# Kernel tuning notes

Measured on AMD Instinct MI355X. Metric: run time of the kernel, lower is better.

The kernel has to match this reference:

```python
import jax, jax.numpy as jnp
import numpy as np

B = 8
A = 3
LEVEL_HW = [(200, 304), (100, 152), (50, 76), (25, 38), (13, 19)]
LEVEL_SIZES = [A * h * w for h, w in LEVEL_HW]  # anchors per level
N_TOTAL = sum(LEVEL_SIZES)                      # 242991
IMG_H, IMG_W = 800.0, 1216.0
PRE_NMS_TOP_N = 2000
POST_NMS_TOP_N = 100
NMS_THRESH = 0.7
MIN_SIZE = 1e-3
BBOX_XFORM_CLIP = float(np.log(1000.0 / 16.0))
NEG = -1e30


def setup_inputs() -> dict:
    key = jax.random.key(0)
    ks = jax.random.split(key, 2 * len(LEVEL_HW) + 3)
    inp = {}
    for i, (h, w) in enumerate(LEVEL_HW):
        inp[f"cls{i}"] = jax.random.normal(ks[2 * i], (B, A, h, w), dtype=jnp.float32)
        inp[f"box{i}"] = jax.random.normal(ks[2 * i + 1], (B, 4 * A, h, w), dtype=jnp.float32) * 0.5
    kc, kw, _ = ks[-3], ks[-2], ks[-1]
    c = jax.random.uniform(kc, (N_TOTAL, 2), dtype=jnp.float32) * jnp.array([IMG_W, IMG_H], jnp.float32)
    wh = 16.0 + jax.random.uniform(kw, (N_TOTAL, 2), dtype=jnp.float32) * 240.0
    inp["anchors"] = jnp.concatenate([c - 0.5 * wh, c + 0.5 * wh], axis=-1)  # x1y1x2y2
    return inp


def _permute_flatten(p, C):
    # [N, A*C, H, W] -> [N, H*W*A, C]  (matches permute_and_flatten)
    n, ac, h, w = p.shape
    a = ac // C
    return p.reshape(n, a, C, h, w).transpose(0, 3, 4, 1, 2).reshape(n, -1, C)


def _decode(deltas, anchors):
    wa = anchors[:, 2] - anchors[:, 0]
    ha = anchors[:, 3] - anchors[:, 1]
    cxa = anchors[:, 0] + 0.5 * wa
    cya = anchors[:, 1] + 0.5 * ha
    dx, dy = deltas[..., 0], deltas[..., 1]
    dw = jnp.minimum(deltas[..., 2], BBOX_XFORM_CLIP)
    dh = jnp.minimum(deltas[..., 3], BBOX_XFORM_CLIP)
    cx = dx * wa + cxa
    cy = dy * ha + cya
    pw = jnp.exp(dw) * wa
    ph = jnp.exp(dh) * ha
    return jnp.stack([cx - 0.5 * pw, cy - 0.5 * ph, cx + 0.5 * pw, cy + 0.5 * ph], axis=-1)


def _nms_single(boxes, scores, lvl, valid):
    # batched_nms: offset boxes by level so cross-level boxes never overlap
    off = lvl.astype(boxes.dtype)[:, None] * (max(IMG_H, IMG_W) + 1.0)
    b0 = boxes + off
    s0 = jnp.where(valid, scores, NEG)  # small-box removal -> impossible to pick
    order = jnp.argsort(-s0)
    b = b0[order]
    s = s0[order]
    areas = (b[:, 2] - b[:, 0]) * (b[:, 3] - b[:, 1])
    suppressed0 = s <= NEG / 2
    idx_range = jnp.arange(s.shape[0])

    def step(suppressed, _):
        avail = jnp.where(suppressed, NEG, s)
        i = jnp.argmax(avail)
        ok = avail[i] > NEG / 2
        bi = b[i]
        xx1 = jnp.maximum(b[:, 0], bi[0])
        yy1 = jnp.maximum(b[:, 1], bi[1])
        xx2 = jnp.minimum(b[:, 2], bi[2])
        yy2 = jnp.minimum(b[:, 3], bi[3])
        inter = jnp.maximum(xx2 - xx1, 0.0) * jnp.maximum(yy2 - yy1, 0.0)
        union = areas + areas[i] - inter
        iou = jnp.where(union > 0, inter / union, 0.0)
        sup_new = suppressed | (iou > NMS_THRESH) | (idx_range == i)
        return jnp.where(ok, sup_new, suppressed), (jnp.where(ok, order[i], 0), ok)

    _, (sel, selv) = jax.lax.scan(step, suppressed0, None, length=POST_NMS_TOP_N)
    out_boxes = jnp.where(selv[:, None], boxes[sel], 0.0)
    out_scores = jnp.where(selv, scores[sel], 0.0)
    return out_boxes, out_scores


def reference(cls0, cls1, cls2, cls3, cls4, box0, box1, box2, box3, box4, anchors):
    cls_levels = [cls0, cls1, cls2, cls3, cls4]
    box_levels = [box0, box1, box2, box3, box4]
    pred_class = jnp.concatenate([_permute_flatten(c, 1) for c in cls_levels], axis=1)  # [B,N,1]
    deltas = jnp.concatenate([_permute_flatten(b, 4) for b in box_levels], axis=1)      # [B,N,4]
    proposals = _decode(deltas, anchors)                                               # [B,N,4]
    scores = pred_class[..., 0]                                                        # [B,N]

    # per-level top-k; replicates the original's cumulative k = min(k, num_anchor)
    keep, lvl = [], []
    k, off = PRE_NMS_TOP_N, 0
    for li, n in enumerate(LEVEL_SIZES):
        k = min(k, n)
        _, idx = jax.lax.top_k(scores[:, off:off + n], k)
        keep.append(idx + off)
        lvl.append(jnp.full((k,), li, dtype=jnp.int32))
        off += n
    keep = jnp.concatenate(keep, axis=1)   # [B,K]
    lvl = jnp.concatenate(lvl)             # [K]

    prop = jnp.take_along_axis(proposals, keep[..., None], axis=1)  # [B,K,4]
    sc = jnp.take_along_axis(scores, keep, axis=1)                  # [B,K]
    prop = jnp.stack([
        jnp.clip(prop[..., 0], 0.0, IMG_W), jnp.clip(prop[..., 1], 0.0, IMG_H),
        jnp.clip(prop[..., 2], 0.0, IMG_W), jnp.clip(prop[..., 3], 0.0, IMG_H)], axis=-1)
    valid = ((prop[..., 2] - prop[..., 0]) >= MIN_SIZE) & ((prop[..., 3] - prop[..., 1]) >= MIN_SIZE)
    boxes_out, scores_out = jax.vmap(lambda bx, s, v: _nms_single(bx, s, lvl, v))(prop, sc, valid)
    return boxes_out, scores_out  # [B,100,4], [B,100]
```

## Files before the change

### kernel.cpp

```cpp
#include <hip/hip_runtime.h>
#include <cstdint>

#define NTOT 242991
#define BATCH 8
#define KTOT 8741
#define CAP 8192
#define NBIN 4096
#define CSTR 16
#define MEMTOT 1943928
#define SLICE 256
#define RSTR 9
#define BCAP 2048
#define NB2 2048
#define DBLK 9

__device__ __forceinline__ int level_of(int n) {
    if (n < 182400) return 0;
    if (n < 228000) return 1;
    if (n < 239400) return 2;
    if (n < 242250) return 3;
    return 4;
}

__device__ __forceinline__ void locate(int n, int& l, int& H, int& W, int& loc) {
    if (n < 182400)      { l = 0; H = 200; W = 304; loc = n; }
    else if (n < 228000) { l = 1; H = 100; W = 152; loc = n - 182400; }
    else if (n < 239400) { l = 2; H = 50;  W = 76;  loc = n - 228000; }
    else if (n < 242250) { l = 3; H = 25;  W = 38;  loc = n - 239400; }
    else                 { l = 4; H = 13;  W = 19;  loc = n - 242250; }
}

__device__ __forceinline__ int classify_bl(int x) {
    int l, HW;
    if (x < 1459200)      { l = 0; HW = 60800; }
    else if (x < 1824000) { l = 1; HW = 15200; x -= 1459200; }
    else if (x < 1915200) { l = 2; HW = 3800;  x -= 1824000; }
    else if (x < 1938000) { l = 3; HW = 950;   x -= 1915200; }
    else                  { l = 4; HW = 247;   x -= 1938000; }
    return (x / (3 * HW)) * 5 + l;
}

__device__ __forceinline__ void mem_decompose(int x, int& b, int& n, int& bl) {
    int HW, off, l;
    if (x < 1459200)      { l = 0; HW = 60800; off = 0; }
    else if (x < 1824000) { l = 1; HW = 15200; off = 182400; x -= 1459200; }
    else if (x < 1915200) { l = 2; HW = 3800;  off = 228000; x -= 1824000; }
    else if (x < 1938000) { l = 3; HW = 950;   off = 239400; x -= 1915200; }
    else                  { l = 4; HW = 247;   off = 242250; x -= 1938000; }
    int seg = 3 * HW;
    b = x / seg; int r = x - b * seg;
    int a = r / HW, pix = r - a * HW;
    n = off + pix * 3 + a;
    bl = b * 5 + l;
}

__device__ __forceinline__ float read_cls(int gid, const float* c0, const float* c1,
                                          const float* c2, const float* c3, const float* c4) {
    return (gid < 1459200) ? c0[gid] :
           (gid < 1824000) ? c1[gid - 1459200] :
           (gid < 1915200) ? c2[gid - 1824000] :
           (gid < 1938000) ? c3[gid - 1915200] : c4[gid - 1938000];
}

__device__ __forceinline__ uint32_t suffix_scan_1024(uint32_t g, uint32_t* lds16, int t) {
    int lane = t & 63, wid = t >> 6;
    uint32_t v = g;
#pragma unroll
    for (int o = 1; o < 64; o <<= 1) {
        uint32_t oth = __shfl_down(v, o, 64);
        if (lane + o < 64) v += oth;
    }
    if (lane == 0) lds16[wid] = v;
    __syncthreads();
    uint32_t w = 0;
    for (int q = wid + 1; q < 16; q++) w += lds16[q];
    __syncthreads();
    return v + w;
}

__device__ __forceinline__ uint32_t prefix_scan_1024(uint32_t g, uint32_t* lds16, int t) {
    int lane = t & 63, wid = t >> 6;
    uint32_t v = g;
#pragma unroll
    for (int o = 1; o < 64; o <<= 1) {
        uint32_t oth = __shfl_up(v, o, 64);
        if (lane >= o) v += oth;
    }
    if (lane == 63) lds16[wid] = v;
    __syncthreads();
    uint32_t w = 0;
    for (int q = 0; q < wid; q++) w += lds16[q];
    __syncthreads();
    return v + w;
}

__device__ __forceinline__ bool iou_hit(float bx1, float by1, float bx2, float by2, float ca,
                                        float4 sv) {
    float xx1 = fmaxf(bx1, sv.x), yy1 = fmaxf(by1, sv.y);
    float xx2 = fminf(bx2, sv.z), yy2 = fminf(by2, sv.w);
    float inter = fmaxf(xx2 - xx1, 0.f) * fmaxf(yy2 - yy1, 0.f);
    float sa = (sv.z - sv.x) * (sv.w - sv.y);
    float un = ca + sa - inter;
    return (un > 0.f) && (inter / un > 0.7f);
}

__global__ __launch_bounds__(1024)
void k_keys(const float* __restrict__ c0, const float* __restrict__ c1,
            const float* __restrict__ c2, const float* __restrict__ c3,
            const float* __restrict__ c4, uint32_t* __restrict__ hist) {
    int t = threadIdx.x;
    int base = blockIdx.x * 1024;
    int gid = base + t;
    bool in = gid < MEMTOT;
    __shared__ uint32_t lh[NBIN];

    int bl = 0, b, n;
    uint32_t u = 0;
    if (in) {
        mem_decompose(gid, b, n, bl);
        float sv = read_cls(gid, c0, c1, c2, c3, c4);
        u = __float_as_uint(sv);
        u ^= (u >> 31) ? 0xFFFFFFFFu : 0x80000000u;
    }
    int blf = classify_bl(base);
    int bll = classify_bl(min(base + 1023, MEMTOT - 1));
    if (blf == bll) {
        for (int j = t; j < NBIN; j += 1024) lh[j] = 0u;
        __syncthreads();
        if (in) atomicAdd(&lh[u >> 20], 1u);
        __syncthreads();
        uint32_t* gh = hist + (size_t)blf * NBIN;
        for (int j = t; j < NBIN; j += 1024) {
            uint32_t v = lh[j];
            if (v) atomicAdd(&gh[j], v);
        }
    } else {
        if (in) atomicAdd(&hist[(size_t)bl * NBIN + (u >> 20)], 1u);
    }
}

__global__ void k_bins(const uint32_t* __restrict__ hist, int* __restrict__ binT,
                       int* __restrict__ rrem) {
    int bl = blockIdx.x;
    const uint32_t* h = hist + (size_t)bl * NBIN;
    int l = bl % 5;
    uint32_t k = (l == 4) ? 741u : 2000u;
    __shared__ uint32_t ts[256];
    __shared__ uint32_t sb[256];
    int t = threadIdx.x;
    uint32_t hh[16];
#pragma unroll
    for (int i = 0; i < 16; i++) hh[i] = h[t * 16 + i];
    uint32_t s = 0;
#pragma unroll
    for (int i = 0; i < 16; i++) s += hh[i];
    ts[t] = s; sb[t] = s;
    __syncthreads();
    for (int d = 1; d < 256; d <<= 1) {
        uint32_t add = (t + d < 256) ? sb[t + d] : 0u;
        __syncthreads();
        sb[t] += add;
        __syncthreads();
    }
    uint32_t inc = sb[t], excl = inc - ts[t];
    if (excl < k && inc >= k) {
        uint32_t cum = excl;
#pragma unroll
        for (int i = 15; i >= 0; i--) {
            if (cum + hh[i] >= k) { binT[bl] = t * 16 + i; rrem[bl] = (int)(k - cum); break; }
            cum += hh[i];
        }
    }
}

__global__ __launch_bounds__(1024)
void k_compact(const float* __restrict__ c0, const float* __restrict__ c1,
               const float* __restrict__ c2, const float* __restrict__ c3,
               const float* __restrict__ c4, const int* __restrict__ binT,
               uint32_t* __restrict__ keep_n, uint32_t* __restrict__ keep_u,
               uint32_t* __restrict__ keep_cnt,
               uint32_t* __restrict__ cand_n, uint32_t* __restrict__ cand_u,
               uint32_t* __restrict__ cand_cnt) {
    int gid = blockIdx.x * 1024 + threadIdx.x;
    bool in = gid < MEMTOT;
    int b = 0, n = 0, bl = 0;
    uint32_t u = 0;
    if (in) {
        mem_decompose(gid, b, n, bl);
        float sv = read_cls(gid, c0, c1, c2, c3, c4);
        u = __float_as_uint(sv);
        u ^= (u >> 31) ? 0xFFFFFFFFu : 0x80000000u;
    }
    int T = in ? binT[bl] : 0x7FFFFFFF;
    int bin = (int)(u >> 20);
    bool pk = in && (bin > T);
    bool pc = in && (bin == T);
    int lane = threadIdx.x & 63;

    unsigned long long act = __ballot(in);
    if (act == 0ull) return;
    int lead = __ffsll(act) - 1;
    int bl0 = __shfl(bl, lead, 64);
    bool unif = (__ballot(in && (bl == bl0)) == act);
    if (unif) {
        int b0 = bl0 / 5, l0 = bl0 % 5;
        uint32_t kbase = (uint32_t)(b0 * KTOT + l0 * 2000);
        unsigned long long mk = __ballot(pk);
        if (mk) {
            int leader = __ffsll(mk) - 1;
            uint32_t bs = 0;
            if (lane == leader) bs = atomicAdd(&keep_cnt[bl0 * CSTR], (uint32_t)__popcll(mk));
            bs = __shfl(bs, leader, 64);
            if (pk) {
                uint32_t p = kbase + bs + (uint32_t)__popcll(mk & ((1ull << lane) - 1ull));
                keep_n[p] = (uint32_t)n; keep_u[p] = u;
            }
        }
        unsigned long long mc = __ballot(pc);
        if (mc) {
            int leader = __ffsll(mc) - 1;
            uint32_t bs = 0;
            if (lane == leader) bs = atomicAdd(&cand_cnt[bl0 * CSTR], (uint32_t)__popcll(mc));
            bs = __shfl(bs, leader, 64);
            if (pc) {
                uint32_t p = bs + (uint32_t)__popcll(mc & ((1ull << lane) - 1ull));
                if (p < CAP) {
                    cand_n[(size_t)bl0 * CAP + p] = (uint32_t)n;
                    cand_u[(size_t)bl0 * CAP + p] = u;
                }
            }
        }
    } else {
        int b1 = bl / 5, l1 = bl % 5;
        if (pk) {
            uint32_t p = atomicAdd(&keep_cnt[bl * CSTR], 1u);
            uint32_t q = (uint32_t)(b1 * KTOT + l1 * 2000) + p;
            keep_n[q] = (uint32_t)n; keep_u[q] = u;
        }
        if (pc) {
            uint32_t p = atomicAdd(&cand_cnt[bl * CSTR], 1u);
            if (p < CAP) {
                cand_n[(size_t)bl * CAP + p] = (uint32_t)n;
                cand_u[(size_t)bl * CAP + p] = u;
            }
        }
    }
}

__global__ __launch_bounds__(1024)
void k_select(const uint32_t* __restrict__ cand_n, const uint32_t* __restrict__ cand_u,
              const uint32_t* __restrict__ cand_cnt, const int* __restrict__ rrem,
              uint32_t* __restrict__ keep_n, uint32_t* __restrict__ keep_u,
              uint32_t* __restrict__ keep_cnt) {
    int bl = blockIdx.x;
    int b = bl / 5, l = bl % 5;
    int C = (int)min(cand_cnt[bl * CSTR], (uint32_t)CAP);
    int r = rrem[bl];
    const uint32_t* cdn = cand_n + (size_t)bl * CAP;
    const uint32_t* cdu = cand_u + (size_t)bl * CAP;
    __shared__ uint32_t hist_l[2048];
    __shared__ uint32_t lds16[16];
    __shared__ unsigned long long pref_sh;
    __shared__ uint32_t kk_sh;
    int t = threadIdx.x;
    if (t == 0) { pref_sh = 0ull; kk_sh = (uint32_t)r; }
    unsigned long long maskAcc = 0ull;
    const int shifts[5] = {41, 30, 19, 8, 0};
    const uint32_t masks[5] = {0x7FFu, 0x7FFu, 0x7FFu, 0x7FFu, 0xFFu};
    __syncthreads();
    for (int p = 0; p < 5; p++) {
        int shift = shifts[p];
        uint32_t msk = masks[p];
        for (int j = t; j < 2048; j += 1024) hist_l[j] = 0u;
        __syncthreads();
        unsigned long long pref = pref_sh;
        uint32_t kk = kk_sh;
        for (int i = t; i < C; i += 1024) {
            unsigned long long key =
                ((unsigned long long)cdu[i] << 32) | (uint32_t)(~cdn[i]);
            if ((key & maskAcc) == pref)
                atomicAdd(&hist_l[(uint32_t)(key >> shift) & msk], 1u);
        }
        __syncthreads();
        uint32_t g = hist_l[2 * t] + hist_l[2 * t + 1];
        uint32_t inc = suffix_scan_1024(g, lds16, t);
        uint32_t excl = inc - g;
        if (excl < kk && inc >= kk) {
            uint32_t hh1 = hist_l[2 * t + 1];
            uint32_t digit, rem;
            if (excl + hh1 >= kk) { digit = 2 * t + 1; rem = kk - excl; }
            else { digit = 2 * t; rem = kk - (excl + hh1); }
            pref_sh = pref | ((unsigned long long)digit << shift);
            kk_sh = rem;
        }
        __syncthreads();
        maskAcc |= (unsigned long long)msk << shift;
    }
    unsigned long long Tk = pref_sh;
    __syncthreads();
    int lane = t & 63;
    for (int i0 = 0; i0 < C; i0 += 1024) {
        int i = i0 + t;
        bool in = i < C;
        uint32_t n = in ? cdn[i] : 0u;
        uint32_t u = in ? cdu[i] : 0u;
        unsigned long long key = in ?
            (((unsigned long long)u << 32) | (uint32_t)(~n)) : 0ull;
        bool pr = in && ((key & maskAcc) >= Tk);
        unsigned long long mk = __ballot(pr);
        if (mk) {
            int leader = __ffsll(mk) - 1;
            uint32_t bs = 0;
            if (lane == leader) bs = atomicAdd(&keep_cnt[bl * CSTR], (uint32_t)__popcll(mk));
            bs = __shfl(bs, leader, 64);
            if (pr) {
                uint32_t p = (uint32_t)(b * KTOT + l * 2000) + bs +
                             (uint32_t)__popcll(mk & ((1ull << lane) - 1ull));
                keep_n[p] = n; keep_u[p] = u;
            }
        }
    }
}

__global__ __launch_bounds__(1024)
void k_decode(const float* __restrict__ b0, const float* __restrict__ b1,
              const float* __restrict__ b2, const float* __restrict__ b3,
              const float* __restrict__ b4, const float* __restrict__ anchors,
              const uint32_t* __restrict__ keep_n, const uint32_t* __restrict__ keep_u,
              float4* __restrict__ nbox, unsigned long long* __restrict__ nkey,
              uint32_t* __restrict__ shist) {
    int blk = blockIdx.x;
    int b = blk / DBLK, seg = blk % DBLK;
    int i = seg * 1024 + threadIdx.x;
    int t = threadIdx.x;
    __shared__ uint32_t lh[NBIN];
    for (int j = t; j < NBIN; j += 1024) lh[j] = 0u;
    __syncthreads();
    if (i < KTOT) {
        int gid = b * KTOT + i;
        int n = (int)keep_n[gid];
        uint32_t u = keep_u[gid];
        int l, H, W, loc; locate(n, l, H, W, loc);
        int a = loc % 3, hw = loc / 3;
        int w = hw % W, h = hw / W;
        const float* bp = (l == 0) ? b0 : (l == 1) ? b1 : (l == 2) ? b2 : (l == 3) ? b3 : b4;
        int HW = H * W;
        int base = ((b * 12 + a * 4) * H + h) * W + w;
        float dx = bp[base], dy = bp[base + HW];
        float dw = bp[base + 2 * HW], dh = bp[base + 3 * HW];
        float ax1 = anchors[4 * n], ay1 = anchors[4 * n + 1];
        float ax2 = anchors[4 * n + 2], ay2 = anchors[4 * n + 3];
        float wa = ax2 - ax1, ha = ay2 - ay1;
        float cxa = ax1 + 0.5f * wa, cya = ay1 + 0.5f * ha;
        const float CLIPV = 4.135166556742356f;
        dw = fminf(dw, CLIPV); dh = fminf(dh, CLIPV);
        float cx = dx * wa + cxa, cy = dy * ha + cya;
        float pw = expf(dw) * wa, ph = expf(dh) * ha;
        float x1 = cx - 0.5f * pw, y1 = cy - 0.5f * ph;
        float x2 = cx + 0.5f * pw, y2 = cy + 0.5f * ph;
        x1 = fminf(fmaxf(x1, 0.f), 1216.f); x2 = fminf(fmaxf(x2, 0.f), 1216.f);
        y1 = fminf(fmaxf(y1, 0.f), 800.f);  y2 = fminf(fmaxf(y2, 0.f), 800.f);
        bool valid = ((x2 - x1) >= 1e-3f) && ((y2 - y1) >= 1e-3f);
        float off = (float)l * 1217.0f;
        nbox[gid] = make_float4(x1 + off, y1 + off, x2 + off, y2 + off);
        nkey[gid] = valid ? (((unsigned long long)u << 32) | (uint32_t)(~n)) : 0ull;
        if (valid) atomicAdd(&lh[u >> 20], 1u);
    }
    __syncthreads();
    uint32_t* gh = shist + (size_t)b * NBIN;
    for (int j = t; j < NBIN; j += 1024) {
        uint32_t v = lh[j];
        if (v) atomicAdd(&gh[j], v);
    }
}

__global__ __launch_bounds__(1024)
void k_nms(const unsigned long long* __restrict__ nkey, const float4* __restrict__ nbox,
           const uint32_t* __restrict__ shist, float* __restrict__ out) {
    int b = blockIdx.x, t = threadIdx.x, lane = t & 63, wid = t >> 6;
    const unsigned long long* NK = nkey + (size_t)b * KTOT;
    const float4* NB = nbox + (size_t)b * KTOT;

    __shared__ unsigned short bstart16[NBIN];
    __shared__ unsigned short bcnt16[NBIN];
    __shared__ unsigned long long k_l[BCAP];
    __shared__ unsigned short p_l[BCAP];
    __shared__ uint32_t scratch[4096];
    __shared__ float4 sel_l[100];
    __shared__ uint32_t sup[SLICE / 32];
    __shared__ uint32_t lds16[16];
    __shared__ uint32_t V_sh, picks_sh, bend_sh, fat_sh;
    __shared__ unsigned long long gmax_sh;
    __shared__ uint32_t jpos_sh;
    __shared__ unsigned long long wred[16];

    const uint32_t* H = shist + (size_t)b * NBIN;
    uint32_t h0 = H[4 * t], h1 = H[4 * t + 1], h2 = H[4 * t + 2], h3 = H[4 * t + 3];
    uint32_t g = h0 + h1 + h2 + h3;
    uint32_t inc = suffix_scan_1024(g, lds16, t);
    if (t == 0) { V_sh = inc; picks_sh = 0u; }
    uint32_t acc = inc - g;
    bstart16[4 * t + 3] = (unsigned short)acc; bcnt16[4 * t + 3] = (unsigned short)h3; acc += h3;
    bstart16[4 * t + 2] = (unsigned short)acc; bcnt16[4 * t + 2] = (unsigned short)h2; acc += h2;
    bstart16[4 * t + 1] = (unsigned short)acc; bcnt16[4 * t + 1] = (unsigned short)h1; acc += h1;
    bstart16[4 * t + 0] = (unsigned short)acc; bcnt16[4 * t + 0] = (unsigned short)h0;
    __syncthreads();

    uint32_t V = V_sh;
    uint32_t picks = 0;
    uint32_t P = 0;
    while (P < V && picks < 100u) {
        uint32_t target = min(P + (uint32_t)BCAP, V);
        if (t == 0) { bend_sh = P; fat_sh = P; }
        __syncthreads();
        {
            uint32_t lmax = P;
            for (int q = t; q < NBIN; q += 1024) {
                uint32_t c = bcnt16[q];
                if (c) {
                    uint32_t s = bstart16[q];
                    if (s >= P && s + c <= target) lmax = max(lmax, s + c);
                    if (s == P) fat_sh = P + c;
                }
            }
#pragma unroll
            for (int o = 32; o > 0; o >>= 1) {
                uint32_t oth = __shfl_down(lmax, o, 64);
                lmax = max(lmax, oth);
            }
            if (lane == 0) atomicMax(&bend_sh, lmax);
        }
        __syncthreads();
        uint32_t B = bend_sh;

        if (B > P) {
            uint32_t total = B - P;
            uint32_t* hist2 = scratch;
            uint32_t* scur2 = scratch + 2048;
            for (int j = t; j < NB2; j += 1024) hist2[j] = 0u;
            __syncthreads();
#pragma unroll
            for (int e = 0; e < DBLK; e++) {
                int i = t + e * 1024;
                if (i < KTOT) {
                    unsigned long long kk = NK[i];
                    if (kk != 0ull) {
                        uint32_t q = (uint32_t)(kk >> 52);
                        uint32_t s = bstart16[q];
                        if (s >= P && s < B) {
                            uint32_t c = bcnt16[q];
                            uint32_t sub = (uint32_t)((kk >> 44) & 0xFFull);
                            uint32_t bin = (s - P) + ((c * (255u - sub)) >> 8);
                            atomicAdd(&hist2[bin], 1u);
                        }
                    }
                }
            }
            __syncthreads();
            uint32_t g0 = hist2[2 * t], g1 = hist2[2 * t + 1];
            uint32_t incp = prefix_scan_1024(g0 + g1, lds16, t);
            uint32_t excl = incp - (g0 + g1);
            scur2[2 * t] = excl; scur2[2 * t + 1] = excl + g0;
            __syncthreads();
#pragma unroll
            for (int e = 0; e < DBLK; e++) {
                int i = t + e * 1024;
                if (i < KTOT) {
                    unsigned long long kk = NK[i];
                    if (kk != 0ull) {
                        uint32_t q = (uint32_t)(kk >> 52);
                        uint32_t s = bstart16[q];
                        if (s >= P && s < B) {
                            uint32_t c = bcnt16[q];
                            uint32_t sub = (uint32_t)((kk >> 44) & 0xFFull);
                            uint32_t bin = (s - P) + ((c * (255u - sub)) >> 8);
                            uint32_t pos = atomicAdd(&scur2[bin], 1u);
                            k_l[pos] = kk; p_l[pos] = (unsigned short)i;
                        }
                    }
                }
            }
            __syncthreads();
#pragma unroll
            for (int qq = 0; qq < 2; qq++) {
                uint32_t bin = 2 * (uint32_t)t + (uint32_t)qq;
                uint32_t c = hist2[bin];
                if (c > 1u) {
                    uint32_t st = scur2[bin] - c;
                    for (uint32_t a = st + 1; a < st + c; a++) {
                        unsigned long long kv = k_l[a]; unsigned short pv = p_l[a];
                        uint32_t w2 = a;
                        while (w2 > st && k_l[w2 - 1] < kv) {
                            k_l[w2] = k_l[w2 - 1]; p_l[w2] = p_l[w2 - 1]; w2--;
                        }
                        k_l[w2] = kv; p_l[w2] = pv;
                    }
                }
            }
            __syncthreads();

            float* box_x = (float*)scratch;
            float* box_y = box_x + SLICE;
            float* box_z = box_y + SLICE;
            float* box_w = box_z + SLICE;
            uint32_t* rows = scratch + 1024;
            for (uint32_t s0 = 0; s0 < total && picks < 100u; s0 += SLICE) {
                uint32_t sl = min((uint32_t)SLICE, total - s0);
                __syncthreads();
                if (t < SLICE) {
                    if (t < (int)sl) {
                        float4 cb = NB[p_l[s0 + t]];
                        box_x[t] = cb.x; box_y[t] = cb.y; box_z[t] = cb.z; box_w[t] = cb.w;
                    } else {
                        box_x[t] = 0.f; box_y[t] = 0.f; box_z[t] = 0.f; box_w[t] = 0.f;
                    }
                }
                if (t < SLICE / 32) sup[t] = 0u;
                __syncthreads();
                if (picks > 0u && t < (int)sl) {
                    float bx1 = box_x[t], by1 = box_y[t], bx2 = box_z[t], by2 = box_w[t];
                    float ca = (bx2 - bx1) * (by2 - by1);
                    bool hit = false;
                    uint32_t s = 0;
                    for (; s + 4 <= picks; s += 4) {
                        float4 v0 = sel_l[s], v1 = sel_l[s + 1], v2 = sel_l[s + 2],
                               v3 = sel_l[s + 3];
                        hit = hit | iou_hit(bx1, by1, bx2, by2, ca, v0)
                                  | iou_hit(bx1, by1, bx2, by2, ca, v1)
                                  | iou_hit(bx1, by1, bx2, by2, ca, v2)
                                  | iou_hit(bx1, by1, bx2, by2, ca, v3);
                    }
                    for (; s < picks; s++) hit = hit | iou_hit(bx1, by1, bx2, by2, ca, sel_l[s]);
                    if (hit) atomicOr(&sup[t >> 5], 1u << (t & 31));
                }
                for (uint32_t widx = t; widx < SLICE * 8; widx += 1024) {
                    uint32_t i = widx & (SLICE - 1);
                    uint32_t wq = widx >> 8;
                    float bx1 = box_x[i], by1 = box_y[i], bx2 = box_z[i], by2 = box_w[i];
                    float ai = (bx2 - bx1) * (by2 - by1);
                    uint32_t jbase = wq * 32u, bits = 0u;
#pragma unroll
                    for (uint32_t qq = 0; qq < 32u; qq++) {
                        uint32_t jj = jbase + qq;
                        float jx1 = box_x[jj], jy1 = box_y[jj],
                              jx2 = box_z[jj], jy2 = box_w[jj];
                        float xx1 = fmaxf(bx1, jx1), yy1 = fmaxf(by1, jy1);
                        float xx2 = fminf(bx2, jx2), yy2 = fminf(by2, jy2);
                        float inter = fmaxf(xx2 - xx1, 0.f) * fmaxf(yy2 - yy1, 0.f);
                        float aj = (jx2 - jx1) * (jy2 - jy1);
                        float un = ai + aj - inter;
                        bool sp = (jj > i) && (un > 0.f) && (inter / un > 0.7f);
                        bits |= ((uint32_t)sp) << qq;
                    }
                    rows[i * RSTR + wq] = bits;
                }
                __syncthreads();
                if (wid == 0) {
                    uint32_t myw = (lane < SLICE / 32) ? sup[lane] : 0u;
                    uint32_t pk = picks;
                    for (uint32_t i = 0; i < sl && pk < 100u; i++) {
                        uint32_t wv = __shfl(myw, (int)(i >> 5), 64);
                        if (!((wv >> (i & 31)) & 1u)) {
                            if (lane < SLICE / 32) myw |= rows[i * RSTR + lane];
                            if (lane == 0) {
                                float4 cb = make_float4(box_x[i], box_y[i], box_z[i], box_w[i]);
                                sel_l[pk] = cb;
                                unsigned long long mkey = k_l[s0 + i];
                                uint32_t n = ~(uint32_t)(mkey & 0xFFFFFFFFull);
                                float off = (float)level_of((int)n) * 1217.0f;
                                float* ob = out + ((size_t)b * 100 + pk) * 4;
                                ob[0] = cb.x - off; ob[1] = cb.y - off;
                                ob[2] = cb.z - off; ob[3] = cb.w - off;
                                uint32_t uu = (uint32_t)(mkey >> 32);
                                uint32_t sb2 = (uu & 0x80000000u) ? (uu ^ 0x80000000u) : ~uu;
                                out[3200 + b * 100 + pk] = __uint_as_float(sb2);
                            }
                            pk++;
                        }
                    }
                    if (lane == 0) picks_sh = pk;
                }
                __syncthreads();
                picks = picks_sh;
            }
            __syncthreads();
        } else {
            B = fat_sh;
            uint32_t cnt = B - P;
            unsigned short Pw = (unsigned short)P;
            unsigned long long last = 0ull;
            bool first = true;
            for (uint32_t done = 0; done < cnt && picks < 100u; done++) {
                unsigned long long lbest = 0ull;
                uint32_t jbest = 0;
                for (uint32_t jj = t; jj < KTOT; jj += 1024) {
                    unsigned long long kk = NK[jj];
                    if (kk != 0ull && bstart16[(uint32_t)(kk >> 52)] == Pw &&
                        (first || kk < last) && kk > lbest) { lbest = kk; jbest = jj; }
                }
                unsigned long long wm = lbest;
#pragma unroll
                for (int o2 = 32; o2 > 0; o2 >>= 1) {
                    unsigned long long oth = __shfl_down(wm, o2, 64);
                    if (oth > wm) wm = oth;
                }
                if (lane == 0) wred[wid] = wm;
                __syncthreads();
                if (t == 0) {
                    unsigned long long mm = wred[0];
                    for (int q = 1; q < 16; q++) if (wred[q] > mm) mm = wred[q];
                    gmax_sh = mm;
                }
                __syncthreads();
                unsigned long long gm = gmax_sh;
                if (gm == 0ull) break;
                if (lbest == gm) jpos_sh = jbest;
                __syncthreads();
                float4 cb = NB[jpos_sh];
                float ca = (cb.z - cb.x) * (cb.w - cb.y);
                bool hit = false;
                for (uint32_t s = (uint32_t)lane; s < picks; s += 64u)
                    hit = hit | iou_hit(cb.x, cb.y, cb.z, cb.w, ca, sel_l[s]);
                bool selq = (__ballot(hit) == 0ull);
                if (selq) {
                    if (t == 0) {
                        sel_l[picks] = cb;
                        uint32_t n = ~(uint32_t)(gm & 0xFFFFFFFFull);
                        float off = (float)level_of((int)n) * 1217.0f;
                        float* ob = out + ((size_t)b * 100 + picks) * 4;
                        ob[0] = cb.x - off; ob[1] = cb.y - off;
                        ob[2] = cb.z - off; ob[3] = cb.w - off;
                        uint32_t uu = (uint32_t)(gm >> 32);
                        uint32_t sb2 = (uu & 0x80000000u) ? (uu ^ 0x80000000u) : ~uu;
                        out[3200 + b * 100 + picks] = __uint_as_float(sb2);
                    }
                    picks++;
                }
                last = gm; first = false;
                __syncthreads();
            }
        }
        P = B;
        __syncthreads();
    }
    for (uint32_t i = picks + (uint32_t)t; i < 100u; i += 1024u) {
        float* ob = out + ((size_t)b * 100 + i) * 4;
        ob[0] = 0.f; ob[1] = 0.f; ob[2] = 0.f; ob[3] = 0.f;
        out[3200 + b * 100 + i] = 0.f;
    }
}

extern "C" void kernel_launch(void* const* d_in, const int* in_sizes, int n_in,
                              void* d_out, int out_size, void* d_ws, size_t ws_size,
                              hipStream_t stream) {
    const float* cls[5] = { (const float*)d_in[0], (const float*)d_in[2], (const float*)d_in[4],
                            (const float*)d_in[6], (const float*)d_in[8] };
    const float* box[5] = { (const float*)d_in[1], (const float*)d_in[3], (const float*)d_in[5],
                            (const float*)d_in[7], (const float*)d_in[9] };
    const float* anchors = (const float*)d_in[10];
    float* out = (float*)d_out;

    uint32_t* W32 = (uint32_t*)d_ws;
    size_t o = 0;
    uint32_t* hist     = W32 + o; o += (size_t)40 * NBIN;
    uint32_t* shist    = W32 + o; o += (size_t)BATCH * NBIN;
    uint32_t* keep_cnt = W32 + o; o += 40 * CSTR;
    uint32_t* cand_cnt = W32 + o; o += 40 * CSTR;
    size_t zero_n = o;
    int*      binT     = (int*)(W32 + o); o += 64;
    int*      rrem     = (int*)(W32 + o); o += 64;
    uint32_t* keep_n   = W32 + o; o += (size_t)BATCH * KTOT;
    uint32_t* keep_u   = W32 + o; o += (size_t)BATCH * KTOT;
    uint32_t* cand_n   = W32 + o; o += (size_t)40 * CAP;
    uint32_t* cand_u   = W32 + o; o += (size_t)40 * CAP;
    o = (o + 3) & ~(size_t)3;
    float4* nbox = (float4*)(W32 + o); o += (size_t)BATCH * KTOT * 4;
    unsigned long long* nkey = (unsigned long long*)(W32 + o); o += (size_t)BATCH * KTOT * 2;

    hipMemsetAsync(d_ws, 0, zero_n * sizeof(uint32_t), stream);
    k_keys<<<(MEMTOT + 1023) / 1024, 1024, 0, stream>>>(cls[0], cls[1], cls[2], cls[3], cls[4],
                                                        hist);
    k_bins<<<40, 256, 0, stream>>>(hist, binT, rrem);
    k_compact<<<(MEMTOT + 1023) / 1024, 1024, 0, stream>>>(cls[0], cls[1], cls[2], cls[3],
                                                           cls[4], binT, keep_n, keep_u,
                                                           keep_cnt, cand_n, cand_u, cand_cnt);
    k_select<<<40, 1024, 0, stream>>>(cand_n, cand_u, cand_cnt, rrem, keep_n, keep_u, keep_cnt);
    k_decode<<<BATCH * DBLK, 1024, 0, stream>>>(box[0], box[1], box[2], box[3], box[4],
                                                anchors, keep_n, keep_u, nbox, nkey, shist);
    k_nms<<<BATCH, 1024, 0, stream>>>(nkey, nbox, shist, out);
}
```

Baseline: 136.3 us.

## Vectorize score and key loads, cache NMS keys in registers, unroll suppression scan

Score reads in the histogram and compaction kernels become float4 loads, with each thread handling four elements and launching 4x fewer blocks. Per-batch keep/box/key buffers are padded to a multiple of four so the decode kernel can use uint4 loads. The NMS kernel keeps its keys in registers instead of re-reading global memory on every pass, and the serial suppression scan drops shuffles in favour of register-held mask words. Together these cut global memory traffic and instruction overhead, at the cost of higher register pressure and fewer resident waves on the score kernels.

```diff
diff --git a/kernel.cpp b/kernel.cpp
--- a/kernel.cpp
+++ b/kernel.cpp
@@ -4,6 +4,7 @@
 #define NTOT 242991
 #define BATCH 8
 #define KTOT 8741
+#define KPAD 8744
 #define CAP 8192
 #define NBIN 4096
 #define CSTR 16
@@ -13,6 +14,8 @@
 #define BCAP 2048
 #define NB2 2048
 #define DBLK 9
+#define DB4 3
+#define KB 475
 
 __device__ __forceinline__ int level_of(int n) {
     if (n < 182400) return 0;
@@ -40,26 +43,14 @@
     return (x / (3 * HW)) * 5 + l;
 }
 
-__device__ __forceinline__ void mem_decompose(int x, int& b, int& n, int& bl) {
-    int HW, off, l;
-    if (x < 1459200)      { l = 0; HW = 60800; off = 0; }
-    else if (x < 1824000) { l = 1; HW = 15200; off = 182400; x -= 1459200; }
-    else if (x < 1915200) { l = 2; HW = 3800;  off = 228000; x -= 1824000; }
-    else if (x < 1938000) { l = 3; HW = 950;   off = 239400; x -= 1915200; }
-    else                  { l = 4; HW = 247;   off = 242250; x -= 1938000; }
-    int seg = 3 * HW;
-    b = x / seg; int r = x - b * seg;
-    int a = r / HW, pix = r - a * HW;
-    n = off + pix * 3 + a;
-    bl = b * 5 + l;
-}
-
-__device__ __forceinline__ float read_cls(int gid, const float* c0, const float* c1,
-                                          const float* c2, const float* c3, const float* c4) {
-    return (gid < 1459200) ? c0[gid] :
-           (gid < 1824000) ? c1[gid - 1459200] :
-           (gid < 1915200) ? c2[gid - 1824000] :
-           (gid < 1938000) ? c3[gid - 1915200] : c4[gid - 1938000];
+__device__ __forceinline__ void level4(int g0, const float* c0, const float* c1,
+                                       const float* c2, const float* c3, const float* c4,
+                                       const float*& cp, int& xx, int& seg, int& off, int& l) {
+    if (g0 < 1459200)      { l = 0; cp = c0; seg = 182400; off = 0;      xx = g0; }
+    else if (g0 < 1824000) { l = 1; cp = c1; seg = 45600;  off = 182400; xx = g0 - 1459200; }
+    else if (g0 < 1915200) { l = 2; cp = c2; seg = 11400;  off = 228000; xx = g0 - 1824000; }
+    else if (g0 < 1938000) { l = 3; cp = c3; seg = 2850;   off = 239400; xx = g0 - 1915200; }
+    else                   { l = 4; cp = c4; seg = 741;    off = 242250; xx = g0 - 1938000; }
 }
 
 __device__ __forceinline__ uint32_t suffix_scan_1024(uint32_t g, uint32_t* lds16, int t) {
@@ -109,25 +100,34 @@
             const float* __restrict__ c2, const float* __restrict__ c3,
             const float* __restrict__ c4, uint32_t* __restrict__ hist) {
     int t = threadIdx.x;
-    int base = blockIdx.x * 1024;
-    int gid = base + t;
-    bool in = gid < MEMTOT;
+    int base = blockIdx.x * 4096;
+    int g0 = base + t * 4;
+    bool in = g0 < MEMTOT;
     __shared__ uint32_t lh[NBIN];
 
-    int bl = 0, b, n;
-    uint32_t u = 0;
+    uint32_t u[4]; int bl[4];
     if (in) {
-        mem_decompose(gid, b, n, bl);
-        float sv = read_cls(gid, c0, c1, c2, c3, c4);
-        u = __float_as_uint(sv);
-        u ^= (u >> 31) ? 0xFFFFFFFFu : 0x80000000u;
+        const float* cp; int xx, seg, off, l;
+        level4(g0, c0, c1, c2, c3, c4, cp, xx, seg, off, l);
+        float4 v = *(const float4*)(cp + xx);
+#pragma unroll
+        for (int e = 0; e < 4; e++) {
+            float sv = (e == 0) ? v.x : (e == 1) ? v.y : (e == 2) ? v.z : v.w;
+            uint32_t uu = __float_as_uint(sv);
+            uu ^= (uu >> 31) ? 0xFFFFFFFFu : 0x80000000u;
+            u[e] = uu;
+            bl[e] = ((xx + e) / seg) * 5 + l;
+        }
     }
     int blf = classify_bl(base);
-    int bll = classify_bl(min(base + 1023, MEMTOT - 1));
+    int bll = classify_bl(min(base + 4095, MEMTOT - 1));
     if (blf == bll) {
         for (int j = t; j < NBIN; j += 1024) lh[j] = 0u;
         __syncthreads();
-        if (in) atomicAdd(&lh[u >> 20], 1u);
+        if (in) {
+#pragma unroll
+            for (int e = 0; e < 4; e++) atomicAdd(&lh[u[e] >> 20], 1u);
+        }
         __syncthreads();
         uint32_t* gh = hist + (size_t)blf * NBIN;
         for (int j = t; j < NBIN; j += 1024) {
@@ -135,7 +135,11 @@
             if (v) atomicAdd(&gh[j], v);
         }
     } else {
-        if (in) atomicAdd(&hist[(size_t)bl * NBIN + (u >> 20)], 1u);
+        if (in) {
+#pragma unroll
+            for (int e = 0; e < 4; e++)
+                atomicAdd(&hist[(size_t)bl[e] * NBIN + (u[e] >> 20)], 1u);
+        }
     }
 }
 
@@ -181,67 +185,89 @@
                uint32_t* __restrict__ keep_cnt,
                uint32_t* __restrict__ cand_n, uint32_t* __restrict__ cand_u,
                uint32_t* __restrict__ cand_cnt) {
-    int gid = blockIdx.x * 1024 + threadIdx.x;
-    bool in = gid < MEMTOT;
-    int b = 0, n = 0, bl = 0;
-    uint32_t u = 0;
+    int t = threadIdx.x;
+    int g0 = blockIdx.x * 4096 + t * 4;
+    bool in = g0 < MEMTOT;
+    int lane = t & 63;
+
+    uint32_t u[4]; int n_[4], bl[4]; bool pk[4], pc[4];
     if (in) {
-        mem_decompose(gid, b, n, bl);
-        float sv = read_cls(gid, c0, c1, c2, c3, c4);
-        u = __float_as_uint(sv);
-        u ^= (u >> 31) ? 0xFFFFFFFFu : 0x80000000u;
-    }
-    int T = in ? binT[bl] : 0x7FFFFFFF;
-    int bin = (int)(u >> 20);
-    bool pk = in && (bin > T);
-    bool pc = in && (bin == T);
-    int lane = threadIdx.x & 63;
+        const float* cp; int xx, seg, off, l;
+        level4(g0, c0, c1, c2, c3, c4, cp, xx, seg, off, l);
+        float4 v = *(const float4*)(cp + xx);
+        int HW = seg / 3;
+#pragma unroll
+        for (int e = 0; e < 4; e++) {
+            float sv = (e == 0) ? v.x : (e == 1) ? v.y : (e == 2) ? v.z : v.w;
+            uint32_t uu = __float_as_uint(sv);
+            uu ^= (uu >> 31) ? 0xFFFFFFFFu : 0x80000000u;
+            u[e] = uu;
+            int xe = xx + e;
+            int b = xe / seg, r = xe - b * seg;
+            int a = r / HW, pix = r - a * HW;
+            n_[e] = off + pix * 3 + a;
+            bl[e] = b * 5 + l;
+        }
+    }
+#pragma unroll
+    for (int e = 0; e < 4; e++) {
+        int T = in ? binT[bl[e]] : 0x7FFFFFFF;
+        int bin = in ? (int)(u[e] >> 20) : 0;
+        pk[e] = in && (bin > T);
+        pc[e] = in && (bin == T);
+    }
 
     unsigned long long act = __ballot(in);
     if (act == 0ull) return;
     int lead = __ffsll(act) - 1;
-    int bl0 = __shfl(bl, lead, 64);
-    bool unif = (__ballot(in && (bl == bl0)) == act);
-    if (unif) {
-        int b0 = bl0 / 5, l0 = bl0 % 5;
-        uint32_t kbase = (uint32_t)(b0 * KTOT + l0 * 2000);
-        unsigned long long mk = __ballot(pk);
-        if (mk) {
-            int leader = __ffsll(mk) - 1;
-            uint32_t bs = 0;
-            if (lane == leader) bs = atomicAdd(&keep_cnt[bl0 * CSTR], (uint32_t)__popcll(mk));
-            bs = __shfl(bs, leader, 64);
-            if (pk) {
-                uint32_t p = kbase + bs + (uint32_t)__popcll(mk & ((1ull << lane) - 1ull));
-                keep_n[p] = (uint32_t)n; keep_u[p] = u;
-            }
-        }
-        unsigned long long mc = __ballot(pc);
-        if (mc) {
-            int leader = __ffsll(mc) - 1;
-            uint32_t bs = 0;
-            if (lane == leader) bs = atomicAdd(&cand_cnt[bl0 * CSTR], (uint32_t)__popcll(mc));
-            bs = __shfl(bs, leader, 64);
-            if (pc) {
-                uint32_t p = bs + (uint32_t)__popcll(mc & ((1ull << lane) - 1ull));
+#pragma unroll
+    for (int e = 0; e < 4; e++) {
+        int bl0 = __shfl(bl[e], lead, 64);
+        bool unif = (__ballot(in && (bl[e] == bl0)) == act);
+        if (unif) {
+            int b0 = bl0 / 5, l0 = bl0 % 5;
+            uint32_t kbase = (uint32_t)(b0 * KPAD + l0 * 2000);
+            unsigned long long mk = __ballot(pk[e]);
+            if (mk) {
+                int leader = __ffsll(mk) - 1;
+                uint32_t bs = 0;
+                if (lane == leader) bs = atomicAdd(&keep_cnt[bl0 * CSTR],
+                                                   (uint32_t)__popcll(mk));
+                bs = __shfl(bs, leader, 64);
+                if (pk[e]) {
+                    uint32_t p = kbase + bs +
+                                 (uint32_t)__popcll(mk & ((1ull << lane) - 1ull));
+                    keep_n[p] = (uint32_t)n_[e]; keep_u[p] = u[e];
+                }
+            }
+            unsigned long long mc = __ballot(pc[e]);
+            if (mc) {
+                int leader = __ffsll(mc) - 1;
+                uint32_t bs = 0;
+                if (lane == leader) bs = atomicAdd(&cand_cnt[bl0 * CSTR],
+                                                   (uint32_t)__popcll(mc));
+                bs = __shfl(bs, leader, 64);
+                if (pc[e]) {
+                    uint32_t p = bs + (uint32_t)__popcll(mc & ((1ull << lane) - 1ull));
+                    if (p < CAP) {
+                        cand_n[(size_t)bl0 * CAP + p] = (uint32_t)n_[e];
+                        cand_u[(size_t)bl0 * CAP + p] = u[e];
+                    }
+                }
+            }
+        } else {
+            if (pk[e]) {
+                int b1 = bl[e] / 5, l1 = bl[e] % 5;
+                uint32_t p = atomicAdd(&keep_cnt[bl[e] * CSTR], 1u);
+                uint32_t q = (uint32_t)(b1 * KPAD + l1 * 2000) + p;
+                keep_n[q] = (uint32_t)n_[e]; keep_u[q] = u[e];
+            }
+            if (pc[e]) {
+                uint32_t p = atomicAdd(&cand_cnt[bl[e] * CSTR], 1u);
                 if (p < CAP) {
-                    cand_n[(size_t)bl0 * CAP + p] = (uint32_t)n;
-                    cand_u[(size_t)bl0 * CAP + p] = u;
-                }
-            }
-        }
-    } else {
-        int b1 = bl / 5, l1 = bl % 5;
-        if (pk) {
-            uint32_t p = atomicAdd(&keep_cnt[bl * CSTR], 1u);
-            uint32_t q = (uint32_t)(b1 * KTOT + l1 * 2000) + p;
-            keep_n[q] = (uint32_t)n; keep_u[q] = u;
-        }
-        if (pc) {
-            uint32_t p = atomicAdd(&cand_cnt[bl * CSTR], 1u);
-            if (p < CAP) {
-                cand_n[(size_t)bl * CAP + p] = (uint32_t)n;
-                cand_u[(size_t)bl * CAP + p] = u;
+                    cand_n[(size_t)bl[e] * CAP + p] = (uint32_t)n_[e];
+                    cand_u[(size_t)bl[e] * CAP + p] = u[e];
+                }
             }
         }
     }
@@ -314,7 +340,7 @@
             if (lane == leader) bs = atomicAdd(&keep_cnt[bl * CSTR], (uint32_t)__popcll(mk));
             bs = __shfl(bs, leader, 64);
             if (pr) {
-                uint32_t p = (uint32_t)(b * KTOT + l * 2000) + bs +
+                uint32_t p = (uint32_t)(b * KPAD + l * 2000) + bs +
                              (uint32_t)__popcll(mk & ((1ull << lane) - 1ull));
                 keep_n[p] = n; keep_u[p] = u;
             }
@@ -330,41 +356,49 @@
               float4* __restrict__ nbox, unsigned long long* __restrict__ nkey,
               uint32_t* __restrict__ shist) {
     int blk = blockIdx.x;
-    int b = blk / DBLK, seg = blk % DBLK;
-    int i = seg * 1024 + threadIdx.x;
+    int b = blk / DB4, seg = blk % DB4;
+    int i0 = seg * 4096 + threadIdx.x * 4;
     int t = threadIdx.x;
     __shared__ uint32_t lh[NBIN];
     for (int j = t; j < NBIN; j += 1024) lh[j] = 0u;
     __syncthreads();
-    if (i < KTOT) {
-        int gid = b * KTOT + i;
-        int n = (int)keep_n[gid];
-        uint32_t u = keep_u[gid];
-        int l, H, W, loc; locate(n, l, H, W, loc);
-        int a = loc % 3, hw = loc / 3;
-        int w = hw % W, h = hw / W;
-        const float* bp = (l == 0) ? b0 : (l == 1) ? b1 : (l == 2) ? b2 : (l == 3) ? b3 : b4;
-        int HW = H * W;
-        int base = ((b * 12 + a * 4) * H + h) * W + w;
-        float dx = bp[base], dy = bp[base + HW];
-        float dw = bp[base + 2 * HW], dh = bp[base + 3 * HW];
-        float ax1 = anchors[4 * n], ay1 = anchors[4 * n + 1];
-        float ax2 = anchors[4 * n + 2], ay2 = anchors[4 * n + 3];
-        float wa = ax2 - ax1, ha = ay2 - ay1;
-        float cxa = ax1 + 0.5f * wa, cya = ay1 + 0.5f * ha;
-        const float CLIPV = 4.135166556742356f;
-        dw = fminf(dw, CLIPV); dh = fminf(dh, CLIPV);
-        float cx = dx * wa + cxa, cy = dy * ha + cya;
-        float pw = expf(dw) * wa, ph = expf(dh) * ha;
-        float x1 = cx - 0.5f * pw, y1 = cy - 0.5f * ph;
-        float x2 = cx + 0.5f * pw, y2 = cy + 0.5f * ph;
-        x1 = fminf(fmaxf(x1, 0.f), 1216.f); x2 = fminf(fmaxf(x2, 0.f), 1216.f);
-        y1 = fminf(fmaxf(y1, 0.f), 800.f);  y2 = fminf(fmaxf(y2, 0.f), 800.f);
-        bool valid = ((x2 - x1) >= 1e-3f) && ((y2 - y1) >= 1e-3f);
-        float off = (float)l * 1217.0f;
-        nbox[gid] = make_float4(x1 + off, y1 + off, x2 + off, y2 + off);
-        nkey[gid] = valid ? (((unsigned long long)u << 32) | (uint32_t)(~n)) : 0ull;
-        if (valid) atomicAdd(&lh[u >> 20], 1u);
+    if (i0 < KTOT) {
+        uint4 kn = *(const uint4*)(keep_n + (size_t)b * KPAD + i0);
+        uint4 ku = *(const uint4*)(keep_u + (size_t)b * KPAD + i0);
+#pragma unroll
+        for (int e = 0; e < 4; e++) {
+            int i = i0 + e;
+            if (i >= KTOT) break;
+            int n = (int)((e == 0) ? kn.x : (e == 1) ? kn.y : (e == 2) ? kn.z : kn.w);
+            uint32_t u = (e == 0) ? ku.x : (e == 1) ? ku.y : (e == 2) ? ku.z : ku.w;
+            int l, H, W, loc; locate(n, l, H, W, loc);
+            int a = loc % 3, hw = loc / 3;
+            int w = hw % W, h = hw / W;
+            const float* bp = (l == 0) ? b0 : (l == 1) ? b1 : (l == 2) ? b2
+                              : (l == 3) ? b3 : b4;
+            int HW = H * W;
+            int base = ((b * 12 + a * 4) * H + h) * W + w;
+            float dx = bp[base], dy = bp[base + HW];
+            float dw = bp[base + 2 * HW], dh = bp[base + 3 * HW];
+            float ax1 = anchors[4 * n], ay1 = anchors[4 * n + 1];
+            float ax2 = anchors[4 * n + 2], ay2 = anchors[4 * n + 3];
+            float wa = ax2 - ax1, ha = ay2 - ay1;
+            float cxa = ax1 + 0.5f * wa, cya = ay1 + 0.5f * ha;
+            const float CLIPV = 4.135166556742356f;
+            dw = fminf(dw, CLIPV); dh = fminf(dh, CLIPV);
+            float cx = dx * wa + cxa, cy = dy * ha + cya;
+            float pw = expf(dw) * wa, ph = expf(dh) * ha;
+            float x1 = cx - 0.5f * pw, y1 = cy - 0.5f * ph;
+            float x2 = cx + 0.5f * pw, y2 = cy + 0.5f * ph;
+            x1 = fminf(fmaxf(x1, 0.f), 1216.f); x2 = fminf(fmaxf(x2, 0.f), 1216.f);
+            y1 = fminf(fmaxf(y1, 0.f), 800.f);  y2 = fminf(fmaxf(y2, 0.f), 800.f);
+            bool valid = ((x2 - x1) >= 1e-3f) && ((y2 - y1) >= 1e-3f);
+            float off = (float)l * 1217.0f;
+            nbox[(size_t)b * KPAD + i] = make_float4(x1 + off, y1 + off, x2 + off, y2 + off);
+            nkey[(size_t)b * KPAD + i] =
+                valid ? (((unsigned long long)u << 32) | (uint32_t)(~n)) : 0ull;
+            if (valid) atomicAdd(&lh[u >> 20], 1u);
+        }
     }
     __syncthreads();
     uint32_t* gh = shist + (size_t)b * NBIN;
@@ -378,8 +412,8 @@
 void k_nms(const unsigned long long* __restrict__ nkey, const float4* __restrict__ nbox,
            const uint32_t* __restrict__ shist, float* __restrict__ out) {
     int b = blockIdx.x, t = threadIdx.x, lane = t & 63, wid = t >> 6;
-    const unsigned long long* NK = nkey + (size_t)b * KTOT;
-    const float4* NB = nbox + (size_t)b * KTOT;
+    const unsigned long long* NK = nkey + (size_t)b * KPAD;
+    const float4* NB = nbox + (size_t)b * KPAD;
 
     __shared__ unsigned short bstart16[NBIN];
     __shared__ unsigned short bcnt16[NBIN];
@@ -394,8 +428,15 @@
     __shared__ uint32_t jpos_sh;
     __shared__ unsigned long long wred[16];
 
-    const uint32_t* H = shist + (size_t)b * NBIN;
-    uint32_t h0 = H[4 * t], h1 = H[4 * t + 1], h2 = H[4 * t + 2], h3 = H[4 * t + 3];
+    unsigned long long rk[DBLK];
+#pragma unroll
+    for (int e = 0; e < DBLK; e++) {
+        int i = t + e * 1024;
+        rk[e] = (i < KTOT) ? NK[i] : 0ull;
+    }
+
+    uint4 hv = ((const uint4*)(shist + (size_t)b * NBIN))[t];
+    uint32_t h0 = hv.x, h1 = hv.y, h2 = hv.z, h3 = hv.w;
     uint32_t g = h0 + h1 + h2 + h3;
     uint32_t inc = suffix_scan_1024(g, lds16, t);
     if (t == 0) { V_sh = inc; picks_sh = 0u; }
@@ -439,20 +480,18 @@
             uint32_t* scur2 = scratch + 2048;
             for (int j = t; j < NB2; j += 1024) hist2[j] = 0u;
             __syncthreads();
+            uint32_t rbin[DBLK];
 #pragma unroll
             for (int e = 0; e < DBLK; e++) {
-                int i = t + e * 1024;
-                if (i < KTOT) {
-                    unsigned long long kk = NK[i];
-                    if (kk != 0ull) {
-                        uint32_t q = (uint32_t)(kk >> 52);
-                        uint32_t s = bstart16[q];
-                        if (s >= P && s < B) {
-                            uint32_t c = bcnt16[q];
-                            uint32_t sub = (uint32_t)((kk >> 44) & 0xFFull);
-                            uint32_t bin = (s - P) + ((c * (255u - sub)) >> 8);
-                            atomicAdd(&hist2[bin], 1u);
-                        }
+                rbin[e] = 0xFFFFFFFFu;
+                if (rk[e] != 0ull) {
+                    uint32_t q = (uint32_t)(rk[e] >> 52);
+                    uint32_t s = bstart16[q];
+                    if (s >= P && s < B) {
+                        uint32_t c = bcnt16[q];
+                        uint32_t sub = (uint32_t)((rk[e] >> 44) & 0xFFull);
+                        rbin[e] = (s - P) + ((c * (255u - sub)) >> 8);
+                        atomicAdd(&hist2[rbin[e]], 1u);
                     }
                 }
             }
@@ -464,20 +503,9 @@
             __syncthreads();
 #pragma unroll
             for (int e = 0; e < DBLK; e++) {
-                int i = t + e * 1024;
-                if (i < KTOT) {
-                    unsigned long long kk = NK[i];
-                    if (kk != 0ull) {
-                        uint32_t q = (uint32_t)(kk >> 52);
-                        uint32_t s = bstart16[q];
-                        if (s >= P && s < B) {
-                            uint32_t c = bcnt16[q];
-                            uint32_t sub = (uint32_t)((kk >> 44) & 0xFFull);
-                            uint32_t bin = (s - P) + ((c * (255u - sub)) >> 8);
-                            uint32_t pos = atomicAdd(&scur2[bin], 1u);
-                            k_l[pos] = kk; p_l[pos] = (unsigned short)i;
-                        }
-                    }
+                if (rbin[e] != 0xFFFFFFFFu) {
+                    uint32_t pos = atomicAdd(&scur2[rbin[e]], 1u);
+                    k_l[pos] = rk[e]; p_l[pos] = (unsigned short)(t + e * 1024);
                 }
             }
             __syncthreads();
@@ -556,28 +584,38 @@
                 }
                 __syncthreads();
                 if (wid == 0) {
-                    uint32_t myw = (lane < SLICE / 32) ? sup[lane] : 0u;
+                    uint32_t w0 = sup[0], w1 = sup[1], w2 = sup[2], w3 = sup[3],
+                             w4 = sup[4], w5 = sup[5], w6 = sup[6], w7 = sup[7];
                     uint32_t pk = picks;
-                    for (uint32_t i = 0; i < sl && pk < 100u; i++) {
-                        uint32_t wv = __shfl(myw, (int)(i >> 5), 64);
-                        if (!((wv >> (i & 31)) & 1u)) {
-                            if (lane < SLICE / 32) myw |= rows[i * RSTR + lane];
-                            if (lane == 0) {
-                                float4 cb = make_float4(box_x[i], box_y[i], box_z[i], box_w[i]);
-                                sel_l[pk] = cb;
-                                unsigned long long mkey = k_l[s0 + i];
-                                uint32_t n = ~(uint32_t)(mkey & 0xFFFFFFFFull);
-                                float off = (float)level_of((int)n) * 1217.0f;
-                                float* ob = out + ((size_t)b * 100 + pk) * 4;
-                                ob[0] = cb.x - off; ob[1] = cb.y - off;
-                                ob[2] = cb.z - off; ob[3] = cb.w - off;
-                                uint32_t uu = (uint32_t)(mkey >> 32);
-                                uint32_t sb2 = (uu & 0x80000000u) ? (uu ^ 0x80000000u) : ~uu;
-                                out[3200 + b * 100 + pk] = __uint_as_float(sb2);
-                            }
-                            pk++;
-                        }
-                    }
+#define SW32(K, WK)                                                                   \
+    for (uint32_t ii = 0; ii < 32u && pk < 100u; ii++) {                              \
+        uint32_t ib = (uint32_t)(K) * 32u + ii;                                       \
+        if (ib >= sl) break;                                                          \
+        if (!((WK >> ii) & 1u)) {                                                     \
+            const uint32_t* rr = &rows[ib * RSTR];                                    \
+            uint32_t r0 = rr[0], r1 = rr[1], r2 = rr[2], r3 = rr[3],                  \
+                     r4 = rr[4], r5 = rr[5], r6 = rr[6], r7 = rr[7];                  \
+            w0 |= r0; w1 |= r1; w2 |= r2; w3 |= r3;                                   \
+            w4 |= r4; w5 |= r5; w6 |= r6; w7 |= r7;                                   \
+            if (lane == 0) {                                                          \
+                float4 cb = make_float4(box_x[ib], box_y[ib], box_z[ib], box_w[ib]);  \
+                sel_l[pk] = cb;                                                       \
+                unsigned long long mkey = k_l[s0 + ib];                               \
+                uint32_t nn = ~(uint32_t)(mkey & 0xFFFFFFFFull);                      \
+                float off = (float)level_of((int)nn) * 1217.0f;                       \
+                float* ob = out + ((size_t)b * 100 + pk) * 4;                         \
+                ob[0] = cb.x - off; ob[1] = cb.y - off;                               \
+                ob[2] = cb.z - off; ob[3] = cb.w - off;                               \
+                uint32_t uu = (uint32_t)(mkey >> 32);                                 \
+                uint32_t sb2 = (uu & 0x80000000u) ? (uu ^ 0x80000000u) : ~uu;         \
+                out[3200 + b * 100 + pk] = __uint_as_float(sb2);                      \
+            }                                                                         \
+            pk++;                                                                     \
+        }                                                                             \
+    }
+                    SW32(0, w0) SW32(1, w1) SW32(2, w2) SW32(3, w3)
+                    SW32(4, w4) SW32(5, w5) SW32(6, w6) SW32(7, w7)
+#undef SW32
                     if (lane == 0) picks_sh = pk;
                 }
                 __syncthreads();
@@ -593,10 +631,13 @@
             for (uint32_t done = 0; done < cnt && picks < 100u; done++) {
                 unsigned long long lbest = 0ull;
                 uint32_t jbest = 0;
-                for (uint32_t jj = t; jj < KTOT; jj += 1024) {
-                    unsigned long long kk = NK[jj];
+#pragma unroll
+                for (int e = 0; e < DBLK; e++) {
+                    unsigned long long kk = rk[e];
                     if (kk != 0ull && bstart16[(uint32_t)(kk >> 52)] == Pw &&
-                        (first || kk < last) && kk > lbest) { lbest = kk; jbest = jj; }
+                        (first || kk < last) && kk > lbest) {
+                        lbest = kk; jbest = (uint32_t)(t + e * 1024);
+                    }
                 }
                 unsigned long long wm = lbest;
 #pragma unroll
@@ -669,23 +710,21 @@
     size_t zero_n = o;
     int*      binT     = (int*)(W32 + o); o += 64;
     int*      rrem     = (int*)(W32 + o); o += 64;
-    uint32_t* keep_n   = W32 + o; o += (size_t)BATCH * KTOT;
-    uint32_t* keep_u   = W32 + o; o += (size_t)BATCH * KTOT;
+    uint32_t* keep_n   = W32 + o; o += (size_t)BATCH * KPAD;
+    uint32_t* keep_u   = W32 + o; o += (size_t)BATCH * KPAD;
     uint32_t* cand_n   = W32 + o; o += (size_t)40 * CAP;
     uint32_t* cand_u   = W32 + o; o += (size_t)40 * CAP;
     o = (o + 3) & ~(size_t)3;
-    float4* nbox = (float4*)(W32 + o); o += (size_t)BATCH * KTOT * 4;
-    unsigned long long* nkey = (unsigned long long*)(W32 + o); o += (size_t)BATCH * KTOT * 2;
+    float4* nbox = (float4*)(W32 + o); o += (size_t)BATCH * KPAD * 4;
+    unsigned long long* nkey = (unsigned long long*)(W32 + o); o += (size_t)BATCH * KPAD * 2;
 
     hipMemsetAsync(d_ws, 0, zero_n * sizeof(uint32_t), stream);
-    k_keys<<<(MEMTOT + 1023) / 1024, 1024, 0, stream>>>(cls[0], cls[1], cls[2], cls[3], cls[4],
-                                                        hist);
+    k_keys<<<KB, 1024, 0, stream>>>(cls[0], cls[1], cls[2], cls[3], cls[4], hist);
     k_bins<<<40, 256, 0, stream>>>(hist, binT, rrem);
-    k_compact<<<(MEMTOT + 1023) / 1024, 1024, 0, stream>>>(cls[0], cls[1], cls[2], cls[3],
-                                                           cls[4], binT, keep_n, keep_u,
-                                                           keep_cnt, cand_n, cand_u, cand_cnt);
+    k_compact<<<KB, 1024, 0, stream>>>(cls[0], cls[1], cls[2], cls[3], cls[4], binT,
+                                       keep_n, keep_u, keep_cnt, cand_n, cand_u, cand_cnt);
     k_select<<<40, 1024, 0, stream>>>(cand_n, cand_u, cand_cnt, rrem, keep_n, keep_u, keep_cnt);
-    k_decode<<<BATCH * DBLK, 1024, 0, stream>>>(box[0], box[1], box[2], box[3], box[4],
-                                                anchors, keep_n, keep_u, nbox, nkey, shist);
+    k_decode<<<BATCH * DB4, 1024, 0, stream>>>(box[0], box[1], box[2], box[3], box[4],
+                                               anchors, keep_n, keep_u, nbox, nkey, shist);
     k_nms<<<BATCH, 1024, 0, stream>>>(nkey, nbox, shist, out);
 }
```

Measured after the change: 144.0 us. 5.6% more time.
